# Performance work log

Hardware: AMD Instinct MI355X
Metric: run time of the kernel (lower is better)

## Reference

```python
import jax, jax.numpy as jnp
import numpy as np

B_, F_, NB, H, R = 32, 10, 20, 128, 2


def setup_inputs() -> dict:
    key = jax.random.key(0)
    ks = jax.random.split(key, 9)
    return {
        "hidden_states": jax.random.normal(ks[0], (B_, F_, NB, H), jnp.float32),
        "cell_states": jax.random.normal(ks[1], (B_, F_, NB, H), jnp.float32),
        "global_t_state": jax.random.normal(ks[2], (B_, NB, H), jnp.float32),
        "global_s_state": jax.random.normal(ks[3], (B_, F_, H), jnp.float32),
        "p": jax.random.normal(ks[4], (B_, F_, NB, H), jnp.float32),
        "U": jax.random.normal(ks[5], (R, F_, NB, 5, H, H), jnp.float32) * 0.05,
        "Wt": jax.random.normal(ks[6], (R, F_, NB, 5, H, H), jnp.float32) * 0.05,
        "Ws": jax.random.normal(ks[7], (R, F_, NB, 5, H, H), jnp.float32) * 0.05,
        "bias": jax.random.normal(ks[8], (R, F_, NB, 5, H), jnp.float32),
    }


def _run_step(h_int, top_h, left_h, top_c, left_c, U_r, Wt_r, Ws_r, b_r):
    # h_int: [B,F,NB,H]; top_*: [B,NB,H]; left_*: [B,F,H]
    # U_r/Wt_r/Ws_r: [F,NB,5,H,H]; b_r: [F,NB,5,H]
    def frame_body(carry, xs):
        h_above, c_above = carry  # [B, NB, H] (row above in the grid)
        x_row, lh, lc, U_f, Wt_f, Ws_f, b_f = xs

        def bone_body(c2, xs2):
            h_left, c_left = c2  # [B, H]
            x, ht, ct, U, Wt, Ws, b = xs2  # U/Wt/Ws: [5,H,H], b: [5,H]
            # 5 gates fused: order (i, f_s, f_t, o, c)
            z = (jnp.einsum('bh,ghk->bgk', x, U)
                 + jnp.einsum('bh,ghk->bgk', ht, Wt)
                 + jnp.einsum('bh,ghk->bgk', h_left, Ws)
                 + b)
            i_n = jax.nn.sigmoid(z[:, 0])
            f_s = jax.nn.sigmoid(z[:, 1])
            f_t = jax.nn.sigmoid(z[:, 2])
            o_n = jax.nn.sigmoid(z[:, 3])
            c_n = jnp.tanh(z[:, 4])
            c_new = i_n * c_n + f_s * c_left + f_t * ct
            h_new = o_n * jnp.tanh(c_new)
            return (h_new, c_new), (h_new, c_new)

        xs2 = (x_row.swapaxes(0, 1), h_above.swapaxes(0, 1),
               c_above.swapaxes(0, 1), U_f, Wt_f, Ws_f, b_f)
        _, (h_row, c_row) = jax.lax.scan(bone_body, (lh, lc), xs2)
        h_row = h_row.swapaxes(0, 1)  # [B, NB, H]
        c_row = c_row.swapaxes(0, 1)
        return (h_row, c_row), (h_row, c_row)

    xs = (h_int.swapaxes(0, 1), left_h.swapaxes(0, 1), left_c.swapaxes(0, 1),
          U_r, Wt_r, Ws_r, b_r)
    _, (h_new, c_new) = jax.lax.scan(frame_body, (top_h, top_c), xs)
    return h_new.swapaxes(0, 1), c_new.swapaxes(0, 1)  # [B,F,NB,H]


def reference(hidden_states, cell_states, global_t_state, global_s_state, p,
              U, Wt, Ws, bias):
    # c-boundaries are identical across recurrent steps
    top_c = jnp.mean(cell_states, axis=1)   # [B, NB, H]
    left_c = jnp.mean(cell_states, axis=2)  # [B, F, H]
    h_int = p
    c_int = jnp.zeros_like(p)
    for i in range(U.shape[0]):  # decoder_recurrent_steps (small, fixed)
        if i == 0:
            h_t, h_s = hidden_states, hidden_states
        elif i == 1:
            h_t = jnp.concatenate([global_t_state[:, None], hidden_states], axis=1)
            h_s = hidden_states
        else:
            h_t = hidden_states
            h_s = jnp.concatenate([global_s_state[:, :, None], hidden_states], axis=2)
        top_h = jnp.mean(h_t, axis=1)   # h[:,0,1:,:]
        left_h = jnp.mean(h_s, axis=2)  # h[:,1:,0,:]
        h_int, c_int = _run_step(h_int, top_h, left_h, top_c, left_c,
                                 U[i], Wt[i], Ws[i], bias[i])
    return h_int, c_int
```

## Files before the change

### kernel.cpp

```cpp
#include <hip/hip_runtime.h>
#include <cstdint>
#include <cstddef>

#define BB  32
#define FF  10
#define NBN 20
#define HH  128
#define GG  5
#define BSTR (FF*NBN*HH)
#define FSTR (NBN*HH)
#define XPAD 132

struct StageList { int cnt; int cells[20]; };

__device__ __forceinline__ float sigm(float x) {
  return 1.f / (1.f + __expf(-x));
}
__device__ __forceinline__ float tanh_fast(float x) {
  float e = __expf(-2.f * fabsf(x));
  float t = (1.f - e) / (1.f + e);
  return copysignf(t, x);
}
__device__ __forceinline__ void fma4(float4& a, const float4 w, const float h) {
  a.x = fmaf(w.x, h, a.x); a.y = fmaf(w.y, h, a.y);
  a.z = fmaf(w.z, h, a.z); a.w = fmaf(w.w, h, a.w);
}
__device__ __forceinline__ void add4(float4& a, const float4 b) {
  a.x += b.x; a.y += b.y; a.z += b.z; a.w += b.w;
}

__global__ void precompute_kernel(
    const float* __restrict__ hid, const float* __restrict__ cell,
    const float* __restrict__ gt,
    float* __restrict__ top_c, float* __restrict__ left_c,
    float* __restrict__ top_h0, float* __restrict__ top_h1,
    float* __restrict__ left_h) {
  int idx = blockIdx.x * 256 + threadIdx.x;
  const int NTOP = BB * NBN * HH;
  const int NLEFT = BB * FF * HH;
  if (idx < NTOP) {
    int h = idx & (HH - 1);
    int n = (idx >> 7) % NBN;
    int b = idx / (HH * NBN);
    const float* hp = hid + (size_t)b * BSTR + n * HH + h;
    const float* cp = cell + (size_t)b * BSTR + n * HH + h;
    float sh = 0.f, sc = 0.f;
#pragma unroll
    for (int f = 0; f < FF; ++f) { sh += hp[f * FSTR]; sc += cp[f * FSTR]; }
    top_c[idx]  = sc * (1.f / FF);
    top_h0[idx] = sh * (1.f / FF);
    top_h1[idx] = (sh + gt[idx]) * (1.f / (FF + 1));
  } else if (idx < NTOP + NLEFT) {
    int j = idx - NTOP;
    int h = j & (HH - 1);
    int f = (j >> 7) % FF;
    int b = j / (HH * FF);
    const float* hp = hid + (size_t)b * BSTR + f * FSTR + h;
    const float* cp = cell + (size_t)b * BSTR + f * FSTR + h;
    float sh = 0.f, sc = 0.f;
#pragma unroll
    for (int n = 0; n < NBN; ++n) { sh += hp[n * HH]; sc += cp[n * HH]; }
    left_c[j] = sc * (1.f / NBN);
    left_h[j] = sh * (1.f / NBN);
  }
}

__global__ __launch_bounds__(256, 4)
void z0_kernel(const float* __restrict__ p, const float* __restrict__ U,
               const float* __restrict__ bias, float* __restrict__ Z) {
  __shared__ __align__(16) float xs[HH][36];
  const int cell = blockIdx.x / GG, g = blockIdx.x % GG;
  const int f = cell / NBN, n = cell % NBN;
  const int t = threadIdx.x;
  const int cid = t & 31, bq = t >> 5;
  const int cellofs = f * FSTR + n * HH;

  for (int i = t; i < BB * HH; i += 256) {
    int b = i >> 7, k = i & (HH - 1);
    xs[k][b] = p[(size_t)b * BSTR + cellofs + k];
  }
  __syncthreads();

  const float* wu = U + (size_t)cell * (GG * HH * HH) + (size_t)g * HH * HH + cid * 4;
  float4 bv = *(const float4*)(bias + (size_t)cell * (GG * HH) + g * HH + cid * 4);
  float4 acc[4];
#pragma unroll
  for (int j = 0; j < 4; ++j) acc[j] = bv;

#pragma unroll 4
  for (int k = 0; k < HH; ++k) {
    float4 w = *(const float4*)(wu + (size_t)k * HH);
    float4 x = *(const float4*)&xs[k][bq * 4];
    fma4(acc[0], w, x.x); fma4(acc[1], w, x.y);
    fma4(acc[2], w, x.z); fma4(acc[3], w, x.w);
  }

  float* zp = Z + (size_t)cell * (BB * GG * HH) + (size_t)g * HH + cid * 4;
#pragma unroll
  for (int j = 0; j < 4; ++j)
    *(float4*)(zp + (size_t)(bq * 4 + j) * (GG * HH)) = acc[j];
}

__global__ __launch_bounds__(256, 2)
void gemv_stage(const float* __restrict__ U, const float* __restrict__ Wt,
                const float* __restrict__ Ws, const float* __restrict__ bias,
                const float* __restrict__ h0, const float* __restrict__ out_h,
                const float* __restrict__ top_h0, const float* __restrict__ top_h1,
                const float* __restrict__ left_h,
                float* __restrict__ Z, StageList sl) {
  __shared__ __align__(16) float xt[3 * BB * XPAD];

  const int cellIdx = blockIdx.x / (GG * 2);
  const int sub = blockIdx.x % (GG * 2);
  const int g = sub >> 1, ch = sub & 1;
  const int packed = sl.cells[cellIdx];
  const int r = (packed >> 16) & 0xff;
  const int f = (packed >> 8) & 0xff;
  const int n = packed & 0xff;
  const int t = threadIdx.x;
  const int cg = t & 15, bq = (t >> 4) & 3, kh = t >> 6;
  const int col = ch * 64 + cg * 4;
  const int cellofs = f * FSTR + n * HH;

  const float* hbase = r ? out_h : h0;
  const float* hp; int hbs;
  if (f > 0) { hp = hbase + cellofs - FSTR; hbs = BSTR; }
  else       { hp = (r ? top_h1 : top_h0) + n * HH; hbs = FSTR; }
  const float* lp; int lbs;
  if (n > 0) { lp = hbase + cellofs - HH; lbs = BSTR; }
  else       { lp = left_h + f * HH; lbs = FF * HH; }

  for (int i = t; i < BB * HH; i += 256) {
    int b = i >> 7, k = i & (HH - 1);
    xt[(0 * BB + b) * XPAD + k] = hp[(size_t)b * hbs + k];
    xt[(1 * BB + b) * XPAD + k] = lp[(size_t)b * lbs + k];
    if (r) xt[(2 * BB + b) * XPAD + k] = h0[(size_t)b * BSTR + cellofs + k];
  }
  __syncthreads();

  const size_t wofs = ((size_t)(r * FF + f) * NBN + n) * ((size_t)GG * HH * HH)
                    + (size_t)g * HH * HH + (size_t)(kh * 32) * HH + col;
  const float* wtp = Wt + wofs;
  const float* wsp = Ws + wofs;
  const float* wup = U + wofs;
  const int ka0 = kh * 32;

  float4 acc[8];
#pragma unroll
  for (int i = 0; i < 8; ++i) acc[i] = make_float4(0.f, 0.f, 0.f, 0.f);

  if (r) {
    for (int kk = 0; kk < 32; kk += 4) {
      float4 wT[4], wS[4], wU[4];
#pragma unroll
      for (int j = 0; j < 4; ++j) {
        wT[j] = *(const float4*)(wtp + (size_t)(kk + j) * HH);
        wS[j] = *(const float4*)(wsp + (size_t)(kk + j) * HH);
        wU[j] = *(const float4*)(wup + (size_t)(kk + j) * HH);
      }
      const int ka = ka0 + kk;
#pragma unroll
      for (int i = 0; i < 8; ++i) {
        const int b = bq + 4 * i;
        float4 xT = *(const float4*)&xt[(0 * BB + b) * XPAD + ka];
        float4 xS = *(const float4*)&xt[(1 * BB + b) * XPAD + ka];
        float4 xU = *(const float4*)&xt[(2 * BB + b) * XPAD + ka];
        float4 a = acc[i];
        fma4(a, wT[0], xT.x); fma4(a, wT[1], xT.y); fma4(a, wT[2], xT.z); fma4(a, wT[3], xT.w);
        fma4(a, wS[0], xS.x); fma4(a, wS[1], xS.y); fma4(a, wS[2], xS.z); fma4(a, wS[3], xS.w);
        fma4(a, wU[0], xU.x); fma4(a, wU[1], xU.y); fma4(a, wU[2], xU.z); fma4(a, wU[3], xU.w);
        acc[i] = a;
      }
    }
  } else {
    for (int kk = 0; kk < 32; kk += 4) {
      float4 wT[4], wS[4];
#pragma unroll
      for (int j = 0; j < 4; ++j) {
        wT[j] = *(const float4*)(wtp + (size_t)(kk + j) * HH);
        wS[j] = *(const float4*)(wsp + (size_t)(kk + j) * HH);
      }
      const int ka = ka0 + kk;
#pragma unroll
      for (int i = 0; i < 8; ++i) {
        const int b = bq + 4 * i;
        float4 xT = *(const float4*)&xt[(0 * BB + b) * XPAD + ka];
        float4 xS = *(const float4*)&xt[(1 * BB + b) * XPAD + ka];
        float4 a = acc[i];
        fma4(a, wT[0], xT.x); fma4(a, wT[1], xT.y); fma4(a, wT[2], xT.z); fma4(a, wT[3], xT.w);
        fma4(a, wS[0], xS.x); fma4(a, wS[1], xS.y); fma4(a, wS[2], xS.z); fma4(a, wS[3], xS.w);
        acc[i] = a;
      }
    }
  }

  __syncthreads();
  const int lane = t & 63;
  if (kh > 0) {
    float* rp = xt + (size_t)((kh - 1) * 64 + lane) * 36;
#pragma unroll
    for (int i = 0; i < 8; ++i) *(float4*)(rp + 4 * i) = acc[i];
  }
  __syncthreads();
  if (kh == 0) {
#pragma unroll
    for (int q = 0; q < 3; ++q) {
      const float* rp = xt + (size_t)(q * 64 + lane) * 36;
#pragma unroll
      for (int i = 0; i < 8; ++i) add4(acc[i], *(const float4*)(rp + 4 * i));
    }

    float* zbase = Z + (size_t)(f * NBN + n) * (BB * GG * HH) + (size_t)g * HH + col;
    if (r) {
      float4 bv = *(const float4*)(bias + (((size_t)(FF + f) * NBN + n) * GG + g) * HH + col);
#pragma unroll
      for (int i = 0; i < 8; ++i) {
        add4(acc[i], bv);
        *(float4*)(zbase + (size_t)(bq + 4 * i) * (GG * HH)) = acc[i];
      }
    } else {
#pragma unroll
      for (int i = 0; i < 8; ++i) {
        float4* dst = (float4*)(zbase + (size_t)(bq + 4 * i) * (GG * HH));
        float4 o = *dst; add4(o, acc[i]); *dst = o;
      }
    }
  }
}

__global__ __launch_bounds__(512)
void combine_stage(const float* __restrict__ Z,
                   const float* __restrict__ top_c, const float* __restrict__ left_c,
                   float* __restrict__ h0, float* __restrict__ c0,
                   float* __restrict__ out_h, float* __restrict__ out_c,
                   StageList sl) {
  const int packed = sl.cells[blockIdx.x];
  const int r = (packed >> 16) & 0xff;
  const int f = (packed >> 8) & 0xff;
  const int n = packed & 0xff;
  const int t = threadIdx.x;
  const int c = t & (HH - 1), bh = t >> 7;
  const int cellofs = f * FSTR + n * HH;

  float* hout = r ? out_h : h0;
  float* cout = r ? out_c : c0;
  const float* ctp; int ctbs;
  if (f > 0) { ctp = cout + cellofs - FSTR; ctbs = BSTR; }
  else       { ctp = top_c + n * HH; ctbs = FSTR; }
  const float* clp; int clbs;
  if (n > 0) { clp = cout + cellofs - HH; clbs = BSTR; }
  else       { clp = left_c + f * HH; clbs = FF * HH; }

  const float* zp = Z + (size_t)(f * NBN + n) * (BB * GG * HH) + c;
#pragma unroll
  for (int j = 0; j < 8; ++j) {
    const int b = bh * 8 + j;
    const float* zb = zp + (size_t)b * (GG * HH);
    float zi = zb[0], zfs = zb[HH], zft = zb[2 * HH], zo = zb[3 * HH], zc = zb[4 * HH];
    float clv = clp[(size_t)b * clbs + c];
    float ctv = ctp[(size_t)b * ctbs + c];
    float iv = sigm(zi), fsv = sigm(zfs), ftv = sigm(zft), ov = sigm(zo);
    float cn = tanh_fast(zc);
    float cnew = fmaf(iv, cn, fmaf(fsv, clv, ftv * ctv));
    float hnew = ov * tanh_fast(cnew);
    hout[(size_t)b * BSTR + cellofs + c] = hnew;
    cout[(size_t)b * BSTR + cellofs + c] = cnew;
  }
}

extern "C" void kernel_launch(void* const* d_in, const int* in_sizes, int n_in,
                              void* d_out, int out_size, void* d_ws, size_t ws_size,
                              hipStream_t stream) {
  const float* hid  = (const float*)d_in[0];
  const float* cell = (const float*)d_in[1];
  const float* gt   = (const float*)d_in[2];
  const float* p    = (const float*)d_in[4];
  const float* U    = (const float*)d_in[5];
  const float* Wt   = (const float*)d_in[6];
  const float* Ws   = (const float*)d_in[7];
  const float* bias = (const float*)d_in[8];

  float* out_h = (float*)d_out;
  float* out_c = out_h + (size_t)BB * BSTR;

  float* w = (float*)d_ws;
  float* h0     = w; w += (size_t)BB * BSTR;
  float* c0     = w; w += (size_t)BB * BSTR;
  float* top_c  = w; w += (size_t)BB * NBN * HH;
  float* left_c = w; w += (size_t)BB * FF * HH;
  float* top_h0 = w; w += (size_t)BB * NBN * HH;
  float* top_h1 = w; w += (size_t)BB * NBN * HH;
  float* left_h = w; w += (size_t)BB * FF * HH;
  float* Z      = w; w += (size_t)FF * NBN * BB * GG * HH;

  const int pre_threads = BB * NBN * HH + BB * FF * HH;
  hipLaunchKernelGGL(precompute_kernel, dim3((pre_threads + 255) / 256), dim3(256),
                     0, stream, hid, cell, gt, top_c, left_c, top_h0, top_h1, left_h);

  hipLaunchKernelGGL(z0_kernel, dim3(FF * NBN * GG), dim3(256), 0, stream,
                     p, U, bias, Z);

  for (int d = 0; d < FF + NBN; ++d) {
    StageList sl; sl.cnt = 0;
    for (int r = 0; r < 2; ++r) {
      int dd = d - r;
      for (int f = 0; f < FF; ++f) {
        int n = dd - f;
        if (n >= 0 && n < NBN) sl.cells[sl.cnt++] = (r << 16) | (f << 8) | n;
      }
    }
    if (sl.cnt == 0) continue;
    hipLaunchKernelGGL(gemv_stage, dim3(sl.cnt * GG * 2), dim3(256), 0, stream,
                       U, Wt, Ws, bias, h0, out_h, top_h0, top_h1, left_h, Z, sl);
    hipLaunchKernelGGL(combine_stage, dim3(sl.cnt), dim3(512), 0, stream,
                       Z, top_c, left_c, h0, c0, out_h, out_c, sl);
  }
}
```

Before: 819.6 us.

## Fuse gate GEMV and LSTM combine into one per-stage kernel using atomic counters

Merges the per-diagonal GEMV kernel and the combine kernel into a single launch. Each of the 10 blocks working on a cell increments a per-cell atomic counter, and the last block to arrive applies the gate nonlinearities and writes h and c. The separate z0 precompute of U·p is removed: the first recurrent step now multiplies by U inline, reading p, so both steps run the same three-weight loop. This halves kernel launches on the serial critical path. In exchange, step-0 cells do more work per stage, and correctness now depends on the atomic acq_rel ordering making other blocks' Z stores visible.

```diff
diff --git a/kernel.cpp b/kernel.cpp
--- a/kernel.cpp
+++ b/kernel.cpp
@@ -10,6 +10,8 @@
 #define BSTR (FF*NBN*HH)
 #define FSTR (NBN*HH)
 #define XPAD 132
+#define NCELLS 400
+#define SC_SYS __HIP_MEMORY_SCOPE_SYSTEM
 
 struct StageList { int cnt; int cells[20]; };
 
@@ -65,61 +67,34 @@
   }
 }
 
-__global__ __launch_bounds__(256, 4)
-void z0_kernel(const float* __restrict__ p, const float* __restrict__ U,
-               const float* __restrict__ bias, float* __restrict__ Z) {
-  __shared__ __align__(16) float xs[HH][36];
-  const int cell = blockIdx.x / GG, g = blockIdx.x % GG;
-  const int f = cell / NBN, n = cell % NBN;
-  const int t = threadIdx.x;
-  const int cid = t & 31, bq = t >> 5;
-  const int cellofs = f * FSTR + n * HH;
-
-  for (int i = t; i < BB * HH; i += 256) {
-    int b = i >> 7, k = i & (HH - 1);
-    xs[k][b] = p[(size_t)b * BSTR + cellofs + k];
-  }
-  __syncthreads();
-
-  const float* wu = U + (size_t)cell * (GG * HH * HH) + (size_t)g * HH * HH + cid * 4;
-  float4 bv = *(const float4*)(bias + (size_t)cell * (GG * HH) + g * HH + cid * 4);
-  float4 acc[4];
-#pragma unroll
-  for (int j = 0; j < 4; ++j) acc[j] = bv;
-
-#pragma unroll 4
-  for (int k = 0; k < HH; ++k) {
-    float4 w = *(const float4*)(wu + (size_t)k * HH);
-    float4 x = *(const float4*)&xs[k][bq * 4];
-    fma4(acc[0], w, x.x); fma4(acc[1], w, x.y);
-    fma4(acc[2], w, x.z); fma4(acc[3], w, x.w);
-  }
-
-  float* zp = Z + (size_t)cell * (BB * GG * HH) + (size_t)g * HH + cid * 4;
-#pragma unroll
-  for (int j = 0; j < 4; ++j)
-    *(float4*)(zp + (size_t)(bq * 4 + j) * (GG * HH)) = acc[j];
-}
-
 __global__ __launch_bounds__(256, 2)
-void gemv_stage(const float* __restrict__ U, const float* __restrict__ Wt,
-                const float* __restrict__ Ws, const float* __restrict__ bias,
-                const float* __restrict__ h0, const float* __restrict__ out_h,
-                const float* __restrict__ top_h0, const float* __restrict__ top_h1,
-                const float* __restrict__ left_h,
-                float* __restrict__ Z, StageList sl) {
+void stage_fused(const float* __restrict__ p,
+                 const float* __restrict__ U,
+                 const float* __restrict__ Wt,
+                 const float* __restrict__ Ws,
+                 const float* __restrict__ bias,
+                 const float* __restrict__ top_c,
+                 const float* __restrict__ left_c,
+                 const float* __restrict__ top_h0,
+                 const float* __restrict__ top_h1,
+                 const float* __restrict__ left_h,
+                 float* __restrict__ h0, float* __restrict__ c0,
+                 float* __restrict__ out_h, float* __restrict__ out_c,
+                 float* __restrict__ Z,
+                 int* __restrict__ zcnt,
+                 StageList sl) {
   __shared__ __align__(16) float xt[3 * BB * XPAD];
-
-  const int cellIdx = blockIdx.x / (GG * 2);
-  const int sub = blockIdx.x % (GG * 2);
+  __shared__ int s_old;
+
+  const int cellIdx = blockIdx.x / 10;
+  const int sub = blockIdx.x % 10;
   const int g = sub >> 1, ch = sub & 1;
   const int packed = sl.cells[cellIdx];
   const int r = (packed >> 16) & 0xff;
   const int f = (packed >> 8) & 0xff;
   const int n = packed & 0xff;
+  const int cid = r * 200 + f * NBN + n;
   const int t = threadIdx.x;
-  const int cg = t & 15, bq = (t >> 4) & 3, kh = t >> 6;
-  const int col = ch * 64 + cg * 4;
   const int cellofs = f * FSTR + n * HH;
 
   const float* hbase = r ? out_h : h0;
@@ -129,15 +104,18 @@
   const float* lp; int lbs;
   if (n > 0) { lp = hbase + cellofs - HH; lbs = BSTR; }
   else       { lp = left_h + f * HH; lbs = FF * HH; }
+  const float* xp = (r ? h0 : p) + cellofs;
 
   for (int i = t; i < BB * HH; i += 256) {
     int b = i >> 7, k = i & (HH - 1);
     xt[(0 * BB + b) * XPAD + k] = hp[(size_t)b * hbs + k];
     xt[(1 * BB + b) * XPAD + k] = lp[(size_t)b * lbs + k];
-    if (r) xt[(2 * BB + b) * XPAD + k] = h0[(size_t)b * BSTR + cellofs + k];
-  }
-  __syncthreads();
-
+    xt[(2 * BB + b) * XPAD + k] = xp[(size_t)b * BSTR + k];
+  }
+  __syncthreads();
+
+  const int cg = t & 15, bq = (t >> 4) & 3, kh = t >> 6;
+  const int col = ch * 64 + cg * 4;
   const size_t wofs = ((size_t)(r * FF + f) * NBN + n) * ((size_t)GG * HH * HH)
                     + (size_t)g * HH * HH + (size_t)(kh * 32) * HH + col;
   const float* wtp = Wt + wofs;
@@ -149,48 +127,26 @@
 #pragma unroll
   for (int i = 0; i < 8; ++i) acc[i] = make_float4(0.f, 0.f, 0.f, 0.f);
 
-  if (r) {
-    for (int kk = 0; kk < 32; kk += 4) {
-      float4 wT[4], wS[4], wU[4];
-#pragma unroll
-      for (int j = 0; j < 4; ++j) {
-        wT[j] = *(const float4*)(wtp + (size_t)(kk + j) * HH);
-        wS[j] = *(const float4*)(wsp + (size_t)(kk + j) * HH);
-        wU[j] = *(const float4*)(wup + (size_t)(kk + j) * HH);
-      }
-      const int ka = ka0 + kk;
-#pragma unroll
-      for (int i = 0; i < 8; ++i) {
-        const int b = bq + 4 * i;
-        float4 xT = *(const float4*)&xt[(0 * BB + b) * XPAD + ka];
-        float4 xS = *(const float4*)&xt[(1 * BB + b) * XPAD + ka];
-        float4 xU = *(const float4*)&xt[(2 * BB + b) * XPAD + ka];
-        float4 a = acc[i];
-        fma4(a, wT[0], xT.x); fma4(a, wT[1], xT.y); fma4(a, wT[2], xT.z); fma4(a, wT[3], xT.w);
-        fma4(a, wS[0], xS.x); fma4(a, wS[1], xS.y); fma4(a, wS[2], xS.z); fma4(a, wS[3], xS.w);
-        fma4(a, wU[0], xU.x); fma4(a, wU[1], xU.y); fma4(a, wU[2], xU.z); fma4(a, wU[3], xU.w);
-        acc[i] = a;
-      }
-    }
-  } else {
-    for (int kk = 0; kk < 32; kk += 4) {
-      float4 wT[4], wS[4];
-#pragma unroll
-      for (int j = 0; j < 4; ++j) {
-        wT[j] = *(const float4*)(wtp + (size_t)(kk + j) * HH);
-        wS[j] = *(const float4*)(wsp + (size_t)(kk + j) * HH);
-      }
-      const int ka = ka0 + kk;
-#pragma unroll
-      for (int i = 0; i < 8; ++i) {
-        const int b = bq + 4 * i;
-        float4 xT = *(const float4*)&xt[(0 * BB + b) * XPAD + ka];
-        float4 xS = *(const float4*)&xt[(1 * BB + b) * XPAD + ka];
-        float4 a = acc[i];
-        fma4(a, wT[0], xT.x); fma4(a, wT[1], xT.y); fma4(a, wT[2], xT.z); fma4(a, wT[3], xT.w);
-        fma4(a, wS[0], xS.x); fma4(a, wS[1], xS.y); fma4(a, wS[2], xS.z); fma4(a, wS[3], xS.w);
-        acc[i] = a;
-      }
+  for (int kk = 0; kk < 32; kk += 4) {
+    float4 wT[4], wS[4], wU[4];
+#pragma unroll
+    for (int j = 0; j < 4; ++j) {
+      wT[j] = *(const float4*)(wtp + (size_t)(kk + j) * HH);
+      wS[j] = *(const float4*)(wsp + (size_t)(kk + j) * HH);
+      wU[j] = *(const float4*)(wup + (size_t)(kk + j) * HH);
+    }
+    const int ka = ka0 + kk;
+#pragma unroll
+    for (int i = 0; i < 8; ++i) {
+      const int b = bq + 4 * i;
+      float4 xT = *(const float4*)&xt[(0 * BB + b) * XPAD + ka];
+      float4 xS = *(const float4*)&xt[(1 * BB + b) * XPAD + ka];
+      float4 xU = *(const float4*)&xt[(2 * BB + b) * XPAD + ka];
+      float4 a = acc[i];
+      fma4(a, wT[0], xT.x); fma4(a, wT[1], xT.y); fma4(a, wT[2], xT.z); fma4(a, wT[3], xT.w);
+      fma4(a, wS[0], xS.x); fma4(a, wS[1], xS.y); fma4(a, wS[2], xS.z); fma4(a, wS[3], xS.w);
+      fma4(a, wU[0], xU.x); fma4(a, wU[1], xU.y); fma4(a, wU[2], xU.z); fma4(a, wU[3], xU.w);
+      acc[i] = a;
     }
   }
 
@@ -209,62 +165,47 @@
 #pragma unroll
       for (int i = 0; i < 8; ++i) add4(acc[i], *(const float4*)(rp + 4 * i));
     }
-
+    float4 bv = *(const float4*)(bias + ((size_t)(r * FF + f) * NBN + n) * (GG * HH)
+                                      + (size_t)g * HH + col);
     float* zbase = Z + (size_t)(f * NBN + n) * (BB * GG * HH) + (size_t)g * HH + col;
-    if (r) {
-      float4 bv = *(const float4*)(bias + (((size_t)(FF + f) * NBN + n) * GG + g) * HH + col);
-#pragma unroll
-      for (int i = 0; i < 8; ++i) {
-        add4(acc[i], bv);
-        *(float4*)(zbase + (size_t)(bq + 4 * i) * (GG * HH)) = acc[i];
-      }
-    } else {
-#pragma unroll
-      for (int i = 0; i < 8; ++i) {
-        float4* dst = (float4*)(zbase + (size_t)(bq + 4 * i) * (GG * HH));
-        float4 o = *dst; add4(o, acc[i]); *dst = o;
-      }
-    }
-  }
-}
-
-__global__ __launch_bounds__(512)
-void combine_stage(const float* __restrict__ Z,
-                   const float* __restrict__ top_c, const float* __restrict__ left_c,
-                   float* __restrict__ h0, float* __restrict__ c0,
-                   float* __restrict__ out_h, float* __restrict__ out_c,
-                   StageList sl) {
-  const int packed = sl.cells[blockIdx.x];
-  const int r = (packed >> 16) & 0xff;
-  const int f = (packed >> 8) & 0xff;
-  const int n = packed & 0xff;
-  const int t = threadIdx.x;
-  const int c = t & (HH - 1), bh = t >> 7;
-  const int cellofs = f * FSTR + n * HH;
-
-  float* hout = r ? out_h : h0;
-  float* cout = r ? out_c : c0;
-  const float* ctp; int ctbs;
-  if (f > 0) { ctp = cout + cellofs - FSTR; ctbs = BSTR; }
-  else       { ctp = top_c + n * HH; ctbs = FSTR; }
-  const float* clp; int clbs;
-  if (n > 0) { clp = cout + cellofs - HH; clbs = BSTR; }
-  else       { clp = left_c + f * HH; clbs = FF * HH; }
-
-  const float* zp = Z + (size_t)(f * NBN + n) * (BB * GG * HH) + c;
-#pragma unroll
-  for (int j = 0; j < 8; ++j) {
-    const int b = bh * 8 + j;
-    const float* zb = zp + (size_t)b * (GG * HH);
-    float zi = zb[0], zfs = zb[HH], zft = zb[2 * HH], zo = zb[3 * HH], zc = zb[4 * HH];
-    float clv = clp[(size_t)b * clbs + c];
-    float ctv = ctp[(size_t)b * ctbs + c];
-    float iv = sigm(zi), fsv = sigm(zfs), ftv = sigm(zft), ov = sigm(zo);
-    float cn = tanh_fast(zc);
-    float cnew = fmaf(iv, cn, fmaf(fsv, clv, ftv * ctv));
-    float hnew = ov * tanh_fast(cnew);
-    hout[(size_t)b * BSTR + cellofs + c] = hnew;
-    cout[(size_t)b * BSTR + cellofs + c] = cnew;
+#pragma unroll
+    for (int i = 0; i < 8; ++i) {
+      add4(acc[i], bv);
+      *(float4*)(zbase + (size_t)(bq + 4 * i) * (GG * HH)) = acc[i];
+    }
+  }
+  __syncthreads();
+
+  if (t == 0)
+    s_old = __hip_atomic_fetch_add(&zcnt[cid], 1, __ATOMIC_ACQ_REL, SC_SYS);
+  __syncthreads();
+
+  if (s_old == 9) {
+    const int c = t & (HH - 1), bh = t >> 7;
+    float* hout = r ? out_h : h0;
+    float* cout = r ? out_c : c0;
+    const float* ctp; int ctbs;
+    if (f > 0) { ctp = cout + cellofs - FSTR; ctbs = BSTR; }
+    else       { ctp = top_c + n * HH; ctbs = FSTR; }
+    const float* clp; int clbs;
+    if (n > 0) { clp = cout + cellofs - HH; clbs = BSTR; }
+    else       { clp = left_c + f * HH; clbs = FF * HH; }
+
+    const float* zp = Z + (size_t)(f * NBN + n) * (BB * GG * HH) + c;
+#pragma unroll
+    for (int j = 0; j < 16; ++j) {
+      const int b = bh * 16 + j;
+      const float* zb = zp + (size_t)b * (GG * HH);
+      float zi = zb[0], zfs = zb[HH], zft = zb[2 * HH], zo = zb[3 * HH], zc = zb[4 * HH];
+      float clv = clp[(size_t)b * clbs + c];
+      float ctv = ctp[(size_t)b * ctbs + c];
+      float iv = sigm(zi), fsv = sigm(zfs), ftv = sigm(zft), ov = sigm(zo);
+      float cn = tanh_fast(zc);
+      float cnew = fmaf(iv, cn, fmaf(fsv, clv, ftv * ctv));
+      float hnew = ov * tanh_fast(cnew);
+      hout[(size_t)b * BSTR + cellofs + c] = hnew;
+      cout[(size_t)b * BSTR + cellofs + c] = cnew;
+    }
   }
 }
 
@@ -292,13 +233,13 @@
   float* top_h1 = w; w += (size_t)BB * NBN * HH;
   float* left_h = w; w += (size_t)BB * FF * HH;
   float* Z      = w; w += (size_t)FF * NBN * BB * GG * HH;
+  int* zcnt = (int*)w;
+
+  hipMemsetAsync(zcnt, 0, NCELLS * sizeof(int), stream);
 
   const int pre_threads = BB * NBN * HH + BB * FF * HH;
   hipLaunchKernelGGL(precompute_kernel, dim3((pre_threads + 255) / 256), dim3(256),
                      0, stream, hid, cell, gt, top_c, left_c, top_h0, top_h1, left_h);
-
-  hipLaunchKernelGGL(z0_kernel, dim3(FF * NBN * GG), dim3(256), 0, stream,
-                     p, U, bias, Z);
 
   for (int d = 0; d < FF + NBN; ++d) {
     StageList sl; sl.cnt = 0;
@@ -310,9 +251,8 @@
       }
     }
     if (sl.cnt == 0) continue;
-    hipLaunchKernelGGL(gemv_stage, dim3(sl.cnt * GG * 2), dim3(256), 0, stream,
-                       U, Wt, Ws, bias, h0, out_h, top_h0, top_h1, left_h, Z, sl);
-    hipLaunchKernelGGL(combine_stage, dim3(sl.cnt), dim3(512), 0, stream,
-                       Z, top_c, left_c, h0, c0, out_h, out_c, sl);
-  }
-}
+    hipLaunchKernelGGL(stage_fused, dim3(sl.cnt * 10), dim3(256), 0, stream,
+                       p, U, Wt, Ws, bias, top_c, left_c, top_h0, top_h1, left_h,
+                       h0, c0, out_h, out_c, Z, zcnt, sl);
+  }
+}
```

After: 855.0 us. +4.3%, slower.
